# Kernel optimization log

Measured on AMD Instinct MI355X. Metric: run time of the kernel, lower is better.

## Reference

```python
import jax, jax.numpy as jnp
import numpy as np

B, S, D, H = 4, 1024, 1024, 16
HD = D // H  # 64
EPS = 1e-5

def _ln(x, g, b):
    m = jnp.mean(x, axis=-1, keepdims=True)
    v = jnp.mean(jnp.square(x - m), axis=-1, keepdims=True)
    return (x - m) * jax.lax.rsqrt(v + EPS) * g + b

def setup_inputs() -> dict:
    key = jax.random.key(0)
    ks = jax.random.split(key, 16)
    std = 0.02
    return {
        "query_tokens": jax.random.normal(ks[0], (B, S, D), jnp.float32),
        "keyvalue_tokens": jax.random.normal(ks[1], (B, S, D), jnp.float32),
        "ln_q_g": jnp.ones((D,), jnp.float32),
        "ln_q_b": jnp.zeros((D,), jnp.float32),
        "ln_kv_g": jnp.ones((D,), jnp.float32),
        "ln_kv_b": jnp.zeros((D,), jnp.float32),
        "Wq": jax.random.normal(ks[2], (2 * D, D), jnp.float32) * std,
        "Wk": jax.random.normal(ks[3], (2 * D, D), jnp.float32) * std,
        "Wv": jax.random.normal(ks[4], (2 * D, D), jnp.float32) * std,
        "Wo": jax.random.normal(ks[5], (D, 2 * D), jnp.float32) * std,
        "lambda_q1": jax.random.normal(ks[6], (HD,), jnp.float32) * 0.1,
        "lambda_k1": jax.random.normal(ks[7], (HD,), jnp.float32) * 0.1,
        "lambda_q2": jax.random.normal(ks[8], (HD,), jnp.float32) * 0.1,
        "lambda_k2": jax.random.normal(ks[9], (HD,), jnp.float32) * 0.1,
        "hn_g": jnp.ones((2 * HD,), jnp.float32),
        "hn_b": jnp.zeros((2 * HD,), jnp.float32),
        "lambda_init": jnp.float32(0.8),
        "disable_second_term": 0,
    }

def reference(query_tokens, keyvalue_tokens, ln_q_g, ln_q_b, ln_kv_g, ln_kv_b,
              Wq, Wk, Wv, Wo, lambda_q1, lambda_k1, lambda_q2, lambda_k2,
              hn_g, hn_b, lambda_init, disable_second_term):
    scale = 1.0 / np.sqrt(HD)
    q_ln = _ln(query_tokens, ln_q_g, ln_q_b)
    kv_ln = _ln(keyvalue_tokens, ln_kv_g, ln_kv_b)
    # projections: torch Linear => x @ W.T ; reshape to [B, H, S, 2*HD]
    def proj(x, W):
        y = jnp.einsum('bsd,ed->bse', x, W)
        return y.reshape(B, S, H, 2 * HD).transpose(0, 2, 1, 3)
    q = proj(q_ln, Wq)
    k = proj(kv_ln, Wk)
    v = proj(kv_ln, Wv)
    q1, q2 = q[..., :HD], q[..., HD:]
    k1, k2 = k[..., :HD], k[..., HD:]
    scores1 = jnp.einsum('bhsd,bhtd->bhst', q1, k1) * scale
    scores2 = jnp.einsum('bhsd,bhtd->bhst', q2, k2) * scale
    attn1 = jax.nn.softmax(scores1, axis=-1)
    attn2 = jax.nn.softmax(scores2, axis=-1)
    if disable_second_term:
        lam = jnp.zeros((), query_tokens.dtype)
    else:
        lam = (jnp.exp(jnp.dot(lambda_q1, lambda_k1))
               - jnp.exp(jnp.dot(lambda_q2, lambda_k2)) + lambda_init)
    out = jnp.einsum('bhst,bhtd->bhsd', attn1 - lam * attn2, v)  # [B,H,S,2HD]
    out = _ln(out, hn_g, hn_b) * (1.0 - lambda_init)
    out = out.transpose(0, 2, 1, 3).reshape(B, S, 2 * D)
    out = jnp.einsum('bse,de->bsd', out, Wo)
    return query_tokens + out
```

## Files before the change

kernel.cpp:

```cpp
#include <hip/hip_runtime.h>
#include <stdint.h>

#define B_  4
#define S_  1024
#define D_  1024
#define H_  16
#define HD_ 64
#define E_  2048
#define C2_ 128

typedef __attribute__((ext_vector_type(8))) short          bf16x8;
typedef __attribute__((ext_vector_type(8))) unsigned short u16x8;
typedef __attribute__((ext_vector_type(4))) unsigned short u16x4;
typedef __attribute__((ext_vector_type(4))) float          f32x4;

#define QSCALE 0.18033688f

__device__ __forceinline__ unsigned short f2bf(float f) {
  union { float f; unsigned int u; } v; v.f = f;
  unsigned int r = v.u + 0x7fffu + ((v.u >> 16) & 1u);
  return (unsigned short)(r >> 16);
}

__device__ __forceinline__ unsigned int cvtpk_bf16(float lo, float hi) {
  unsigned int r;
  asm("v_cvt_pk_bf16_f32 %0, %1, %2" : "=v"(r) : "v"(lo), "v"(hi));
  return r;
}

__device__ __forceinline__ float red16_sum(float x) {
  x += __int_as_float(__builtin_amdgcn_mov_dpp(__float_as_int(x), 0xB1, 0xF, 0xF, false));
  x += __int_as_float(__builtin_amdgcn_mov_dpp(__float_as_int(x), 0x4E, 0xF, 0xF, false));
  x += __int_as_float(__builtin_amdgcn_mov_dpp(__float_as_int(x), 0x141, 0xF, 0xF, false));
  x += __int_as_float(__builtin_amdgcn_mov_dpp(__float_as_int(x), 0x140, 0xF, 0xF, false));
  return x;
}

typedef const __attribute__((address_space(1))) unsigned int* gas1_t;
typedef __attribute__((address_space(3))) unsigned int* las3_t;
__device__ __forceinline__ void gload16(const void* g, void* s) {
  __builtin_amdgcn_global_load_lds((gas1_t)g, (las3_t)s, 16, 0, 0);
}

__global__ __launch_bounds__(256) void ln_cast_k(const float* __restrict__ x,
                                                 const float* __restrict__ g,
                                                 const float* __restrict__ bb,
                                                 unsigned short* __restrict__ out) {
  int row = blockIdx.x;
  int tid = threadIdx.x;
  const float* xr = x + (size_t)row * D_;
  float4 xv = *(const float4*)(xr + tid * 4);
  float s  = xv.x + xv.y + xv.z + xv.w;
  float sq = xv.x * xv.x + xv.y * xv.y + xv.z * xv.z + xv.w * xv.w;
#pragma unroll
  for (int m = 32; m; m >>= 1) { s += __shfl_xor(s, m, 64); sq += __shfl_xor(sq, m, 64); }
  __shared__ float ps[4], pq[4];
  int w = tid >> 6, l = tid & 63;
  if (l == 0) { ps[w] = s; pq[w] = sq; }
  __syncthreads();
  s  = ps[0] + ps[1] + ps[2] + ps[3];
  sq = pq[0] + pq[1] + pq[2] + pq[3];
  float mean = s * (1.f / D_);
  float var  = sq * (1.f / D_) - mean * mean;
  float rstd = rsqrtf(var + 1e-5f);
  float4 gv = *(const float4*)(g + tid * 4);
  float4 bv = *(const float4*)(bb + tid * 4);
  u16x4 o;
  o.x = f2bf((xv.x - mean) * rstd * gv.x + bv.x);
  o.y = f2bf((xv.y - mean) * rstd * gv.y + bv.y);
  o.z = f2bf((xv.z - mean) * rstd * gv.z + bv.z);
  o.w = f2bf((xv.w - mean) * rstd * gv.w + bv.w);
  *(u16x4*)(out + (size_t)row * D_ + tid * 4) = o;
}

__global__ __launch_bounds__(256) void cast_k(const float* __restrict__ in,
                                              unsigned short* __restrict__ out, int n4) {
  int i = blockIdx.x * 256 + threadIdx.x;
  if (i < n4) {
    float4 v = *(const float4*)(in + (size_t)i * 4);
    u16x4 o; o.x = f2bf(v.x); o.y = f2bf(v.y); o.z = f2bf(v.z); o.w = f2bf(v.w);
    *(u16x4*)(out + (size_t)i * 4) = o;
  }
}

__global__ __launch_bounds__(256) void gemm_proj_k(
    const unsigned short* __restrict__ qln, const unsigned short* __restrict__ kvln,
    const unsigned short* __restrict__ Wq,  const unsigned short* __restrict__ Wk,
    const unsigned short* __restrict__ Wv,
    unsigned short* __restrict__ qb, unsigned short* __restrict__ kb,
    unsigned short* __restrict__ vtb) {
  const int K = D_;
  int which = blockIdx.z;
  const unsigned short* A = (which == 0) ? qln : kvln;
  const unsigned short* W = (which == 0) ? Wq : (which == 1 ? Wk : Wv);
  unsigned short* O = (which == 0) ? qb : (which == 1 ? kb : vtb);
  int m0 = blockIdx.y * 128, n0 = blockIdx.x * 128;
  __shared__ __align__(16) char psm[128 * 272];
  char* lsA = psm;
  char* lsB = psm + 16384;
  int tid = threadIdx.x, l = tid & 63, w = tid >> 6;
  int wm = (w >> 1) * 64, wn = (w & 1) * 64;
  f32x4 acc[4][4] = {};
  for (int kt = 0; kt < K; kt += 64) {
    __syncthreads();
#pragma unroll
    for (int i = 0; i < 4; i++) {
      int rbase = (i * 4 + w) * 8;
      int row = rbase + (l >> 3), c8 = l & 7;
      int sc = (c8 ^ (row & 7)) * 8;
      gload16(A + (size_t)(m0 + row) * K + kt + sc, lsA + rbase * 128);
      gload16(W + (size_t)(n0 + row) * K + kt + sc, lsB + rbase * 128);
    }
    __syncthreads();
#pragma unroll
    for (int kk = 0; kk < 2; kk++) {
      bf16x8 af[4], bfr[4];
      int koff = kk * 64 + (l >> 4) * 16;
#pragma unroll
      for (int mf = 0; mf < 4; mf++) {
        int row = wm + mf * 16 + (l & 15);
        af[mf] = *(const bf16x8*)(lsA + row * 128 + (koff ^ ((row & 7) << 4)));
      }
#pragma unroll
      for (int nf = 0; nf < 4; nf++) {
        int row = wn + nf * 16 + (l & 15);
        bfr[nf] = *(const bf16x8*)(lsB + row * 128 + (koff ^ ((row & 7) << 4)));
      }
#pragma unroll
      for (int mf = 0; mf < 4; mf++)
#pragma unroll
        for (int nf = 0; nf < 4; nf++)
          acc[mf][nf] = __builtin_amdgcn_mfma_f32_16x16x32_bf16(af[mf], bfr[nf], acc[mf][nf], 0, 0, 0);
    }
  }
  if (which < 2) {
    float sc = (which == 0) ? QSCALE : 1.0f;
#pragma unroll
    for (int mf = 0; mf < 4; mf++)
#pragma unroll
      for (int nf = 0; nf < 4; nf++)
#pragma unroll
        for (int r = 0; r < 4; r++) {
          int gm = m0 + wm + mf * 16 + (l >> 4) * 4 + r;
          int gn = n0 + wn + nf * 16 + (l & 15);
          int b = gm >> 10, s = gm & 1023;
          int h = gn >> 7,  c = gn & 127;
          O[((size_t)((b * H_ + h) * S_ + s)) * C2_ + c] = f2bf(acc[mf][nf][r] * sc);
        }
  } else {
    __syncthreads();
#pragma unroll
    for (int mf = 0; mf < 4; mf++)
#pragma unroll
      for (int nf = 0; nf < 4; nf++) {
        int crow = wn + nf * 16 + (l & 15);
        int sloc = wm + mf * 16 + (l >> 4) * 4;
        u16x4 pk4;
        pk4.x = f2bf(acc[mf][nf][0]); pk4.y = f2bf(acc[mf][nf][1]);
        pk4.z = f2bf(acc[mf][nf][2]); pk4.w = f2bf(acc[mf][nf][3]);
        *(u16x4*)(psm + (size_t)crow * 272 + sloc * 2) = pk4;
      }
    __syncthreads();
    int b = m0 >> 10, sbase = m0 & 1023;
#pragma unroll
    for (int i = 0; i < 8; i++) {
      int u2 = i * 256 + tid;
      int row = u2 >> 4, c16 = u2 & 15;
      u16x8 vv = *(const u16x8*)(psm + (size_t)row * 272 + c16 * 16);
      int gn = n0 + row, h = gn >> 7, cfeat = gn & 127;
      *(u16x8*)(O + ((size_t)((b * H_ + h) * C2_ + cfeat)) * S_ + sbase + c16 * 8) = vv;
    }
  }
}

__global__ __launch_bounds__(256) void gemm_out_k(
    const unsigned short* __restrict__ A, const unsigned short* __restrict__ W,
    const float* __restrict__ resid, float* __restrict__ out) {
  const int K = E_;
  int m0 = blockIdx.y * 128, n0 = blockIdx.x * 128;
  __shared__ __align__(16) char psm2[32768];
  char* lsA = psm2;
  char* lsB = psm2 + 16384;
  int tid = threadIdx.x, l = tid & 63, w = tid >> 6;
  int wm = (w >> 1) * 64, wn = (w & 1) * 64;
  f32x4 acc[4][4] = {};
  for (int kt = 0; kt < K; kt += 64) {
    __syncthreads();
#pragma unroll
    for (int i = 0; i < 4; i++) {
      int rbase = (i * 4 + w) * 8;
      int row = rbase + (l >> 3), c8 = l & 7;
      int sc = (c8 ^ (row & 7)) * 8;
      gload16(A + (size_t)(m0 + row) * K + kt + sc, lsA + rbase * 128);
      gload16(W + (size_t)(n0 + row) * K + kt + sc, lsB + rbase * 128);
    }
    __syncthreads();
#pragma unroll
    for (int kk = 0; kk < 2; kk++) {
      bf16x8 af[4], bfr[4];
      int koff = kk * 64 + (l >> 4) * 16;
#pragma unroll
      for (int mf = 0; mf < 4; mf++) {
        int row = wm + mf * 16 + (l & 15);
        af[mf] = *(const bf16x8*)(lsA + row * 128 + (koff ^ ((row & 7) << 4)));
      }
#pragma unroll
      for (int nf = 0; nf < 4; nf++) {
        int row = wn + nf * 16 + (l & 15);
        bfr[nf] = *(const bf16x8*)(lsB + row * 128 + (koff ^ ((row & 7) << 4)));
      }
#pragma unroll
      for (int mf = 0; mf < 4; mf++)
#pragma unroll
        for (int nf = 0; nf < 4; nf++)
          acc[mf][nf] = __builtin_amdgcn_mfma_f32_16x16x32_bf16(af[mf], bfr[nf], acc[mf][nf], 0, 0, 0);
    }
  }
#pragma unroll
  for (int mf = 0; mf < 4; mf++)
#pragma unroll
    for (int nf = 0; nf < 4; nf++)
#pragma unroll
      for (int r = 0; r < 4; r++) {
        int gm = m0 + wm + mf * 16 + (l >> 4) * 4 + r;
        int gn = n0 + wn + nf * 16 + (l & 15);
        size_t idx = (size_t)gm * D_ + gn;
        out[idx] = acc[mf][nf][r] + resid[idx];
      }
}

__global__ __launch_bounds__(256, 2) void attn_k(
    const unsigned short* __restrict__ q, const unsigned short* __restrict__ k,
    const unsigned short* __restrict__ vt,
    const float* __restrict__ lq1, const float* __restrict__ lk1,
    const float* __restrict__ lq2, const float* __restrict__ lk2,
    const float* __restrict__ hng, const float* __restrict__ hnb,
    const float* __restrict__ lambda_init, const int* __restrict__ dis2,
    unsigned short* __restrict__ out) {
  int bh = blockIdx.x;
  int qt = blockIdx.y;
  int tid = threadIdx.x, ln = tid & 63, w = tid >> 6;
  int g = ln >> 4, c = ln & 15;
  bool godd = (g & 1);
  __shared__ unsigned short lsK[2][64 * 128];
  __shared__ unsigned short lsVt[2][128 * 64];
  __shared__ float s_lam, s_osc;

  if (tid < 64) {
    float a = lq1[ln] * lk1[ln];
    float cc = lq2[ln] * lk2[ln];
#pragma unroll
    for (int m = 32; m; m >>= 1) { a += __shfl_xor(a, m, 64); cc += __shfl_xor(cc, m, 64); }
    if (ln == 0) {
      float li = lambda_init[0];
      float lam = __expf(a) - __expf(cc) + li;
      if (dis2[0] != 0) lam = 0.f;
      s_lam = lam;
      s_osc = 1.f - li;
    }
  }

  const unsigned short* kbh = k + (size_t)bh * S_ * C2_;
  const unsigned short* vbh = vt + (size_t)bh * C2_ * S_;

  bf16x8 qf[2][2][2];
#pragma unroll
  for (int sub = 0; sub < 2; sub++) {
    int qrow = qt * 128 + w * 32 + sub * 16 + c;
    const unsigned short* qrp = q + ((size_t)bh * S_ + qrow) * C2_;
#pragma unroll
    for (int t = 0; t < 2; t++)
#pragma unroll
      for (int kk = 0; kk < 2; kk++)
        qf[sub][t][kk] = *(const bf16x8*)(qrp + t * 64 + kk * 32 + g * 8);
  }

  f32x4 lones[2][2] = {};
  f32x4 o[2][2][8] = {};
  bf16x8 onesf;
#pragma unroll
  for (int j = 0; j < 8; j++) onesf[j] = (short)0x3F80;

#define STAGE_KV(buf, t0s)                                                            \
  {                                                                                   \
    const unsigned short* kbase = kbh + (size_t)(t0s) * C2_;                          \
    _Pragma("unroll")                                                                 \
    for (int i = 0; i < 4; i++) {                                                     \
      int rb = w * 16 + i * 4;                                                        \
      int row = rb + (ln >> 4), c16 = ln & 15;                                        \
      gload16(kbase + row * C2_ + ((c16 ^ (row & 7)) * 8),                            \
              (char*)&lsK[buf][0] + rb * 256);                                        \
    }                                                                                 \
    const unsigned short* vbase = vbh + (t0s);                                        \
    _Pragma("unroll")                                                                 \
    for (int i = 0; i < 4; i++) {                                                     \
      int rb = w * 32 + i * 8;                                                        \
      int row = rb + (ln >> 3), c8 = ln & 7;                                          \
      gload16(vbase + (size_t)row * S_ + ((c8 ^ (row & 7)) * 8),                      \
              (char*)&lsVt[buf][0] + rb * 128);                                       \
    }                                                                                 \
  }

  STAGE_KV(0, 0);
  __syncthreads();

  for (int it = 0; it < S_ / 64; ++it) {
    int cur = it & 1;
    if (it + 1 < S_ / 64) STAGE_KV(cur ^ 1, (it + 1) * 64);

    unsigned int paw[2][2][2][4];

#pragma unroll
    for (int term = 0; term < 2; term++) {
      f32x4 sf[2][4] = {};
      __builtin_amdgcn_s_setprio(1);
#pragma unroll
      for (int kk = 0; kk < 2; kk++) {
#pragma unroll
        for (int nf = 0; nf < 4; nf++) {
          int kfrow = nf * 16 + c;
          bf16x8 kf = *(const bf16x8*)((char*)&lsK[cur][0] + kfrow * 256 +
                        ((term * 128 + kk * 64 + g * 16) ^ ((kfrow & 7) << 4)));
          sf[0][nf] = __builtin_amdgcn_mfma_f32_16x16x32_bf16(kf, qf[0][term][kk], sf[0][nf], 0, 0, 0);
          sf[1][nf] = __builtin_amdgcn_mfma_f32_16x16x32_bf16(kf, qf[1][term][kk], sf[1][nf], 0, 0, 0);
        }
      }
      __builtin_amdgcn_s_setprio(0);
#pragma unroll
      for (int sub = 0; sub < 2; sub++) {
#pragma unroll
        for (int nf = 0; nf < 4; nf++)
#pragma unroll
          for (int r = 0; r < 4; r++)
            sf[sub][nf][r] = exp2f(sf[sub][nf][r]);
#pragma unroll
        for (int kk = 0; kk < 2; kk++) {
          unsigned int X0 = cvtpk_bf16(sf[sub][2 * kk][0], sf[sub][2 * kk][1]);
          unsigned int X1 = cvtpk_bf16(sf[sub][2 * kk][2], sf[sub][2 * kk][3]);
          unsigned int Y0 = cvtpk_bf16(sf[sub][2 * kk + 1][0], sf[sub][2 * kk + 1][1]);
          unsigned int Y1 = cvtpk_bf16(sf[sub][2 * kk + 1][2], sf[sub][2 * kk + 1][3]);
          asm("v_permlane32_swap_b32 %0, %1" : "+v"(X0), "+v"(Y0));
          asm("v_permlane32_swap_b32 %0, %1" : "+v"(X1), "+v"(Y1));
          unsigned int t0w = __shfl_xor((int)Y0, 16), u0 = __shfl_xor((int)X0, 16);
          unsigned int t1w = __shfl_xor((int)Y1, 16), u1 = __shfl_xor((int)X1, 16);
          paw[sub][term][kk][0] = godd ? t0w : X0;
          paw[sub][term][kk][1] = godd ? t1w : X1;
          paw[sub][term][kk][2] = godd ? Y0 : u0;
          paw[sub][term][kk][3] = godd ? Y1 : u1;
        }
      }
    }

#pragma unroll
    for (int kk = 0; kk < 2; kk++) {
      union { unsigned int u[4]; bf16x8 v; } pa[2][2];
#pragma unroll
      for (int sub = 0; sub < 2; sub++)
#pragma unroll
        for (int term = 0; term < 2; term++)
#pragma unroll
          for (int j = 0; j < 4; j++) pa[sub][term].u[j] = paw[sub][term][kk][j];
      __builtin_amdgcn_s_setprio(1);
#pragma unroll
      for (int sub = 0; sub < 2; sub++) {
        lones[sub][0] = __builtin_amdgcn_mfma_f32_16x16x32_bf16(pa[sub][0].v, onesf, lones[sub][0], 0, 0, 0);
        lones[sub][1] = __builtin_amdgcn_mfma_f32_16x16x32_bf16(pa[sub][1].v, onesf, lones[sub][1], 0, 0, 0);
      }
#pragma unroll
      for (int nf2 = 0; nf2 < 8; nf2++) {
        int vrow = nf2 * 16 + c;
        bf16x8 vf = *(const bf16x8*)((char*)&lsVt[cur][0] + vrow * 128 +
                      ((kk * 64 + g * 16) ^ ((vrow & 7) << 4)));
#pragma unroll
        for (int sub = 0; sub < 2; sub++) {
          o[sub][0][nf2] = __builtin_amdgcn_mfma_f32_16x16x32_bf16(pa[sub][0].v, vf, o[sub][0][nf2], 0, 0, 0);
          o[sub][1][nf2] = __builtin_amdgcn_mfma_f32_16x16x32_bf16(pa[sub][1].v, vf, o[sub][1][nf2], 0, 0, 0);
        }
      }
      __builtin_amdgcn_s_setprio(0);
    }
    __syncthreads();
  }

  float lam = s_lam, osc = s_osc;
  int b = bh >> 4, h = bh & 15;
#pragma unroll
  for (int sub = 0; sub < 2; sub++)
#pragma unroll
    for (int r = 0; r < 4; r++) {
      float inv1 = 1.f / lones[sub][0][r];
      float inv2 = lam / lones[sub][1][r];
      float vals[8];
      float sum = 0.f, sq = 0.f;
#pragma unroll
      for (int nf2 = 0; nf2 < 8; nf2++) {
        float vv = o[sub][0][nf2][r] * inv1 - o[sub][1][nf2][r] * inv2;
        vals[nf2] = vv;
        sum += vv; sq += vv * vv;
      }
      sum = red16_sum(sum);
      sq  = red16_sum(sq);
      float mean = sum * (1.f / 128.f);
      float var  = sq * (1.f / 128.f) - mean * mean;
      float rstd = rsqrtf(var + 1e-5f);
      int srow = qt * 128 + w * 32 + sub * 16 + g * 4 + r;
      unsigned short* orow = out + ((size_t)(b * S_ + srow)) * E_ + h * C2_;
#pragma unroll
      for (int nf2 = 0; nf2 < 8; nf2++) {
        int feat = nf2 * 16 + c;
        float y = (vals[nf2] - mean) * rstd * hng[feat] + hnb[feat];
        orow[feat] = f2bf(y * osc);
      }
    }
}

extern "C" void kernel_launch(void* const* d_in, const int* in_sizes, int n_in,
                              void* d_out, int out_size, void* d_ws, size_t ws_size,
                              hipStream_t stream) {
  const float* qtok = (const float*)d_in[0];
  const float* kvtok = (const float*)d_in[1];
  const float* lnqg = (const float*)d_in[2];
  const float* lnqb = (const float*)d_in[3];
  const float* lnkg = (const float*)d_in[4];
  const float* lnkb = (const float*)d_in[5];
  const float* Wq = (const float*)d_in[6];
  const float* Wk = (const float*)d_in[7];
  const float* Wv = (const float*)d_in[8];
  const float* Wo = (const float*)d_in[9];
  const float* lq1 = (const float*)d_in[10];
  const float* lk1 = (const float*)d_in[11];
  const float* lq2 = (const float*)d_in[12];
  const float* lk2 = (const float*)d_in[13];
  const float* hng = (const float*)d_in[14];
  const float* hnb = (const float*)d_in[15];
  const float* lami = (const float*)d_in[16];
  const int*   dis2 = (const int*)d_in[17];
  float* outp = (float*)d_out;

  char* ws = (char*)d_ws;
  const size_t MB = 1024 * 1024;
  unsigned short* qln    = (unsigned short*)(ws + 0);
  unsigned short* kvln   = (unsigned short*)(ws + 8 * MB);
  unsigned short* attn_o = (unsigned short*)(ws + 0);
  unsigned short* Wqb = (unsigned short*)(ws + 16 * MB);
  unsigned short* Wkb = (unsigned short*)(ws + 20 * MB);
  unsigned short* Wvb = (unsigned short*)(ws + 24 * MB);
  unsigned short* Wob = (unsigned short*)(ws + 28 * MB);
  unsigned short* qb  = (unsigned short*)(ws + 32 * MB);
  unsigned short* kb  = (unsigned short*)(ws + 48 * MB);
  unsigned short* vtb = (unsigned short*)(ws + 64 * MB);

  ln_cast_k<<<dim3(4096), dim3(256), 0, stream>>>(qtok, lnqg, lnqb, qln);
  ln_cast_k<<<dim3(4096), dim3(256), 0, stream>>>(kvtok, lnkg, lnkb, kvln);
  cast_k<<<dim3(2048), dim3(256), 0, stream>>>(Wq, Wqb, 512 * 1024);
  cast_k<<<dim3(2048), dim3(256), 0, stream>>>(Wk, Wkb, 512 * 1024);
  cast_k<<<dim3(2048), dim3(256), 0, stream>>>(Wv, Wvb, 512 * 1024);
  cast_k<<<dim3(2048), dim3(256), 0, stream>>>(Wo, Wob, 512 * 1024);
  gemm_proj_k<<<dim3(16, 32, 3), dim3(256), 0, stream>>>(qln, kvln, Wqb, Wkb, Wvb, qb, kb, vtb);
  attn_k<<<dim3(64, 8), dim3(256), 0, stream>>>(qb, kb, vtb, lq1, lk1, lq2, lk2,
                                                hng, hnb, lami, dis2, attn_o);
  gemm_out_k<<<dim3(8, 32), dim3(256), 0, stream>>>(attn_o, Wob, qtok, outp);
}
```

Before: 222.8 us.

## Fuse preprocessing launches and single-buffer attention KV with permlane16 swaps

```diff
diff --git a/kernel.cpp b/kernel.cpp
--- a/kernel.cpp
+++ b/kernel.cpp
@@ -42,12 +42,36 @@
   __builtin_amdgcn_global_load_lds((gas1_t)g, (las3_t)s, 16, 0, 0);
 }
 
-__global__ __launch_bounds__(256) void ln_cast_k(const float* __restrict__ x,
-                                                 const float* __restrict__ g,
-                                                 const float* __restrict__ bb,
-                                                 unsigned short* __restrict__ out) {
+__global__ __launch_bounds__(256) void pre_k(const float* __restrict__ xq,
+                                             const float* __restrict__ xkv,
+                                             const float* __restrict__ gq,
+                                             const float* __restrict__ bq,
+                                             const float* __restrict__ gkv,
+                                             const float* __restrict__ bkv,
+                                             unsigned short* __restrict__ oq,
+                                             unsigned short* __restrict__ okv,
+                                             const float* __restrict__ w0, const float* __restrict__ w1,
+                                             const float* __restrict__ w2, const float* __restrict__ w3,
+                                             unsigned short* __restrict__ wo0, unsigned short* __restrict__ wo1,
+                                             unsigned short* __restrict__ wo2, unsigned short* __restrict__ wo3) {
+  int y = blockIdx.y;
+  int tid = threadIdx.x;
+  if (y >= 2) {
+    int i = blockIdx.x * 256 + tid;
+    if (i >= 512 * 1024) return;
+    int sel = y - 2;
+    const float* in = (sel == 0) ? w0 : (sel == 1) ? w1 : (sel == 2) ? w2 : w3;
+    unsigned short* out = (sel == 0) ? wo0 : (sel == 1) ? wo1 : (sel == 2) ? wo2 : wo3;
+    float4 v = *(const float4*)(in + (size_t)i * 4);
+    u16x4 o; o.x = f2bf(v.x); o.y = f2bf(v.y); o.z = f2bf(v.z); o.w = f2bf(v.w);
+    *(u16x4*)(out + (size_t)i * 4) = o;
+    return;
+  }
+  const float* x = y ? xkv : xq;
+  const float* g = y ? gkv : gq;
+  const float* bb = y ? bkv : bq;
+  unsigned short* out = y ? okv : oq;
   int row = blockIdx.x;
-  int tid = threadIdx.x;
   const float* xr = x + (size_t)row * D_;
   float4 xv = *(const float4*)(xr + tid * 4);
   float s  = xv.x + xv.y + xv.z + xv.w;
@@ -71,16 +95,6 @@
   o.z = f2bf((xv.z - mean) * rstd * gv.z + bv.z);
   o.w = f2bf((xv.w - mean) * rstd * gv.w + bv.w);
   *(u16x4*)(out + (size_t)row * D_ + tid * 4) = o;
-}
-
-__global__ __launch_bounds__(256) void cast_k(const float* __restrict__ in,
-                                              unsigned short* __restrict__ out, int n4) {
-  int i = blockIdx.x * 256 + threadIdx.x;
-  if (i < n4) {
-    float4 v = *(const float4*)(in + (size_t)i * 4);
-    u16x4 o; o.x = f2bf(v.x); o.y = f2bf(v.y); o.z = f2bf(v.z); o.w = f2bf(v.w);
-    *(u16x4*)(out + (size_t)i * 4) = o;
-  }
 }
 
 __global__ __launch_bounds__(256) void gemm_proj_k(
@@ -229,7 +243,7 @@
       }
 }
 
-__global__ __launch_bounds__(256, 2) void attn_k(
+__global__ __launch_bounds__(256, 1) void attn_k(
     const unsigned short* __restrict__ q, const unsigned short* __restrict__ k,
     const unsigned short* __restrict__ vt,
     const float* __restrict__ lq1, const float* __restrict__ lk1,
@@ -241,9 +255,8 @@
   int qt = blockIdx.y;
   int tid = threadIdx.x, ln = tid & 63, w = tid >> 6;
   int g = ln >> 4, c = ln & 15;
-  bool godd = (g & 1);
-  __shared__ unsigned short lsK[2][64 * 128];
-  __shared__ unsigned short lsVt[2][128 * 64];
+  __shared__ unsigned short lsK[64 * 128];
+  __shared__ unsigned short lsVt[128 * 64];
   __shared__ float s_lam, s_osc;
 
   if (tid < 64) {
@@ -281,7 +294,7 @@
 #pragma unroll
   for (int j = 0; j < 8; j++) onesf[j] = (short)0x3F80;
 
-#define STAGE_KV(buf, t0s)                                                            \
+#define STAGE_KV(t0s)                                                                 \
   {                                                                                   \
     const unsigned short* kbase = kbh + (size_t)(t0s) * C2_;                          \
     _Pragma("unroll")                                                                 \
@@ -289,7 +302,7 @@
       int rb = w * 16 + i * 4;                                                        \
       int row = rb + (ln >> 4), c16 = ln & 15;                                        \
       gload16(kbase + row * C2_ + ((c16 ^ (row & 7)) * 8),                            \
-              (char*)&lsK[buf][0] + rb * 256);                                        \
+              (char*)&lsK[0] + rb * 256);                                             \
     }                                                                                 \
     const unsigned short* vbase = vbh + (t0s);                                        \
     _Pragma("unroll")                                                                 \
@@ -297,16 +310,13 @@
       int rb = w * 32 + i * 8;                                                        \
       int row = rb + (ln >> 3), c8 = ln & 7;                                          \
       gload16(vbase + (size_t)row * S_ + ((c8 ^ (row & 7)) * 8),                      \
-              (char*)&lsVt[buf][0] + rb * 128);                                       \
+              (char*)&lsVt[0] + rb * 128);                                            \
     }                                                                                 \
   }
 
-  STAGE_KV(0, 0);
-  __syncthreads();
-
-  for (int it = 0; it < S_ / 64; ++it) {
-    int cur = it & 1;
-    if (it + 1 < S_ / 64) STAGE_KV(cur ^ 1, (it + 1) * 64);
+  for (int t0 = 0; t0 < S_; t0 += 64) {
+    STAGE_KV(t0);
+    __syncthreads();
 
     unsigned int paw[2][2][2][4];
 
@@ -319,7 +329,7 @@
 #pragma unroll
         for (int nf = 0; nf < 4; nf++) {
           int kfrow = nf * 16 + c;
-          bf16x8 kf = *(const bf16x8*)((char*)&lsK[cur][0] + kfrow * 256 +
+          bf16x8 kf = *(const bf16x8*)((char*)&lsK[0] + kfrow * 256 +
                         ((term * 128 + kk * 64 + g * 16) ^ ((kfrow & 7) << 4)));
           sf[0][nf] = __builtin_amdgcn_mfma_f32_16x16x32_bf16(kf, qf[0][term][kk], sf[0][nf], 0, 0, 0);
           sf[1][nf] = __builtin_amdgcn_mfma_f32_16x16x32_bf16(kf, qf[1][term][kk], sf[1][nf], 0, 0, 0);
@@ -341,12 +351,10 @@
           unsigned int Y1 = cvtpk_bf16(sf[sub][2 * kk + 1][2], sf[sub][2 * kk + 1][3]);
           asm("v_permlane32_swap_b32 %0, %1" : "+v"(X0), "+v"(Y0));
           asm("v_permlane32_swap_b32 %0, %1" : "+v"(X1), "+v"(Y1));
-          unsigned int t0w = __shfl_xor((int)Y0, 16), u0 = __shfl_xor((int)X0, 16);
-          unsigned int t1w = __shfl_xor((int)Y1, 16), u1 = __shfl_xor((int)X1, 16);
-          paw[sub][term][kk][0] = godd ? t0w : X0;
-          paw[sub][term][kk][1] = godd ? t1w : X1;
-          paw[sub][term][kk][2] = godd ? Y0 : u0;
-          paw[sub][term][kk][3] = godd ? Y1 : u1;
+          asm("v_permlane16_swap_b32 %0, %1" : "+v"(X0), "+v"(Y0));
+          asm("v_permlane16_swap_b32 %0, %1" : "+v"(X1), "+v"(Y1));
+          paw[sub][term][kk][0] = X0; paw[sub][term][kk][1] = X1;
+          paw[sub][term][kk][2] = Y0; paw[sub][term][kk][3] = Y1;
         }
       }
     }
@@ -369,7 +377,7 @@
 #pragma unroll
       for (int nf2 = 0; nf2 < 8; nf2++) {
         int vrow = nf2 * 16 + c;
-        bf16x8 vf = *(const bf16x8*)((char*)&lsVt[cur][0] + vrow * 128 +
+        bf16x8 vf = *(const bf16x8*)((char*)&lsVt[0] + vrow * 128 +
                       ((kk * 64 + g * 16) ^ ((vrow & 7) << 4)));
 #pragma unroll
         for (int sub = 0; sub < 2; sub++) {
@@ -450,12 +458,8 @@
   unsigned short* kb  = (unsigned short*)(ws + 48 * MB);
   unsigned short* vtb = (unsigned short*)(ws + 64 * MB);
 
-  ln_cast_k<<<dim3(4096), dim3(256), 0, stream>>>(qtok, lnqg, lnqb, qln);
-  ln_cast_k<<<dim3(4096), dim3(256), 0, stream>>>(kvtok, lnkg, lnkb, kvln);
-  cast_k<<<dim3(2048), dim3(256), 0, stream>>>(Wq, Wqb, 512 * 1024);
-  cast_k<<<dim3(2048), dim3(256), 0, stream>>>(Wk, Wkb, 512 * 1024);
-  cast_k<<<dim3(2048), dim3(256), 0, stream>>>(Wv, Wvb, 512 * 1024);
-  cast_k<<<dim3(2048), dim3(256), 0, stream>>>(Wo, Wob, 512 * 1024);
+  pre_k<<<dim3(4096, 6), dim3(256), 0, stream>>>(qtok, kvtok, lnqg, lnqb, lnkg, lnkb, qln, kvln,
+                                                 Wq, Wk, Wv, Wo, Wqb, Wkb, Wvb, Wob);
   gemm_proj_k<<<dim3(16, 32, 3), dim3(256), 0, stream>>>(qln, kvln, Wqb, Wkb, Wvb, qb, kb, vtb);
   attn_k<<<dim3(64, 8), dim3(256), 0, stream>>>(qb, kb, vtb, lq1, lk1, lq2, lk2,
                                                 hng, hnb, lami, dis2, attn_o);
```

New measurement: 229.2 us. +2.9%, slower.
